# Kernel optimization log

Measured on AMD Instinct MI355X. Metric: run time of the kernel, lower is better.

The kernel has to match this reference:

```python
import jax, jax.numpy as jnp
import numpy as np

# graph layout constants
B = 64        # number of graphs
NPG = 512     # nodes per graph
N = B * NPG   # total nodes
DEG = 16      # avg degree
E = N * DEG   # total edges
F_IN = 256
H, C = 4, 64  # heads, per-head dim
K = NPG // 2  # topk pooling keeps ratio=0.5 per graph


def setup_inputs() -> dict:
    key = jax.random.key(0)
    ks = jax.random.split(key, 8)
    x = jax.random.normal(ks[0], (N, F_IN), dtype=jnp.float32)
    # within-graph random edges (src -> dst), contiguous node ids per graph
    offs = jnp.repeat(jnp.arange(B, dtype=jnp.int64) * NPG, NPG * DEG)
    src = offs + jax.random.randint(ks[1], (E,), 0, NPG)
    dst = offs + jax.random.randint(ks[2], (E,), 0, NPG)
    edge_index = jnp.stack([src, dst]).astype(jnp.int64)
    W = jax.random.normal(ks[3], (F_IN, H, C), dtype=jnp.float32) / np.sqrt(F_IN)
    att_src = jax.random.normal(ks[4], (H, C), dtype=jnp.float32) / np.sqrt(C)
    att_dst = jax.random.normal(ks[5], (H, C), dtype=jnp.float32) / np.sqrt(C)
    bias = jnp.zeros((H * C,), dtype=jnp.float32)
    bn_gamma = jnp.ones((H * C,), dtype=jnp.float32)
    bn_beta = jnp.zeros((H * C,), dtype=jnp.float32)
    pool_weight = jax.random.normal(ks[6], (H * C,), dtype=jnp.float32) / np.sqrt(H * C)
    return {"x": x, "edge_index": edge_index, "W": W, "att_src": att_src,
            "att_dst": att_dst, "bias": bias, "bn_gamma": bn_gamma,
            "bn_beta": bn_beta, "pool_weight": pool_weight}


def reference(x, edge_index, W, att_src, att_dst, bias, bn_gamma, bn_beta, pool_weight):
    n = x.shape[0]
    # --- GATConv ---
    h = jnp.einsum('nf,fhc->nhc', x, W)                 # [N,H,C]
    a_src = jnp.sum(h * att_src, axis=-1)               # [N,H]
    a_dst = jnp.sum(h * att_dst, axis=-1)               # [N,H]
    loops = jnp.arange(n, dtype=edge_index.dtype)        # add_self_loops=True default
    src = jnp.concatenate([edge_index[0], loops])
    dst = jnp.concatenate([edge_index[1], loops])
    e = jax.nn.leaky_relu(a_src[src] + a_dst[dst], 0.2)  # [E+N,H]
    # scatter-softmax over edges grouped by destination node
    emax = jax.ops.segment_max(e, dst, num_segments=n)
    ex = jnp.exp(e - emax[dst])
    den = jax.ops.segment_sum(ex, dst, num_segments=n)
    alpha = ex / (den[dst] + 1e-16)                      # [E+N,H]
    msg = alpha[:, :, None] * h[src]                     # [E+N,H,C]
    out = jax.ops.segment_sum(msg, dst, num_segments=n)  # [N,H,C]
    feat = out.reshape(n, H * C) + bias                  # concat heads
    # --- ReLU + BatchNorm (batch stats, training mode) ---
    feat = jax.nn.relu(feat)
    mean = jnp.mean(feat, axis=0)
    var = jnp.var(feat, axis=0)
    feat = (feat - mean) * jax.lax.rsqrt(var + 1e-5) * bn_gamma + bn_beta
    # --- TopKPooling (score = x.w/||w||, keep top ratio per graph, gate by tanh) ---
    score = feat @ pool_weight / jnp.linalg.norm(pool_weight)  # [N]
    top_s, top_i = jax.lax.top_k(score.reshape(B, NPG), K)     # [B,K]
    fg = feat.reshape(B, NPG, H * C)
    sel = jnp.take_along_axis(fg, top_i[:, :, None], axis=1)    # [B,K,HC]
    pooled = sel * jnp.tanh(top_s)[:, :, None]
    return pooled.reshape(B * K, H * C)
```

## Files before the change

kernel.cpp:

```cpp
#include <hip/hip_runtime.h>
#include <math.h>

#define N_NODES 32768
#define NPG 512
#define NGRAPH 64
#define KKEEP 256
#define CAP 64

typedef __attribute__((ext_vector_type(8))) short short8;
typedef __attribute__((ext_vector_type(4))) float f32x4;

__device__ __forceinline__ unsigned short f2bf(float v) {
  unsigned u = __builtin_bit_cast(unsigned, v);
  u = (u + 0x7FFFu + ((u >> 16) & 1u)) >> 16;
  return (unsigned short)u;
}
__device__ __forceinline__ float bf2f(unsigned short u) {
  unsigned v = ((unsigned)u) << 16;
  return __builtin_bit_cast(float, v);
}

__device__ __forceinline__ void async_cp16(unsigned short* l, const unsigned short* g) {
  __builtin_amdgcn_global_load_lds(
      (const __attribute__((address_space(1))) unsigned int*)g,
      (__attribute__((address_space(3))) unsigned int*)l, 16, 0, 0);
}

__device__ __forceinline__ void block_barrier() {
  __builtin_amdgcn_sched_barrier(0);
  asm volatile("s_barrier" ::: "memory");
  __builtin_amdgcn_sched_barrier(0);
}
__device__ __forceinline__ void wait_all() {
  asm volatile("s_waitcnt vmcnt(0) lgkmcnt(0)" ::: "memory");
  __builtin_amdgcn_sched_barrier(0);
}

__global__ __launch_bounds__(256) void k_conv(
    const float* __restrict__ W,
    unsigned short* __restrict__ wth, unsigned short* __restrict__ wtl,
    unsigned short* __restrict__ wtll) {
  const int t = threadIdx.x;
  int n = blockIdx.x * 4 + (t >> 6);
  int k = (t & 63) * 4;
  unsigned short hb[4], lb[4], qb[4];
#pragma unroll
  for (int j = 0; j < 4; j++) {
    float v = W[(size_t)(k + j) * 256 + n];
    unsigned short hh = f2bf(v);
    float e1 = v - bf2f(hh);
    unsigned short ll = f2bf(e1);
    float e2 = e1 - bf2f(ll);
    hb[j] = hh; lb[j] = ll; qb[j] = f2bf(e2);
  }
  *(uint2*)&wth[(size_t)n * 256 + k] = *(uint2*)&hb[0];
  *(uint2*)&wtl[(size_t)n * 256 + k] = *(uint2*)&lb[0];
  *(uint2*)&wtll[(size_t)n * 256 + k] = *(uint2*)&qb[0];
}

#define A_STR 129
#define A_SZ 12384
#define B_BASE 12384
#define B_SZ 12288
__global__ __launch_bounds__(512, 4) void k_gemm_hist(
    const float* __restrict__ x,
    const unsigned short* __restrict__ wth, const unsigned short* __restrict__ wtl,
    const unsigned short* __restrict__ wtll,
    const float* __restrict__ attS, const float* __restrict__ attD,
    float* __restrict__ h, float* __restrict__ a_src, float* __restrict__ a_dst,
    const int* __restrict__ ei, int E, int* __restrict__ cnt,
    unsigned short* __restrict__ nbr) {
  __shared__ unsigned short lds[36960];
  const int t = threadIdx.x;
  const int bid = blockIdx.x;
  if (bid >= 512) {
    int e = (bid - 512) * 512 + t;
    if (e < E) {
      int s = ei[e];
      int d = ei[E + e];
      int slot = atomicAdd(&cnt[d], 1);
      if (slot < CAP) nbr[(size_t)d * CAP + slot] = (unsigned short)(s & (NPG - 1));
    }
    return;
  }
  const int mb = (bid & 7) * 32 + (bid >> 4);
  const int nh = (bid >> 3) & 1;
  const int row0 = mb * 128;
  const int wid = t >> 6, lane = t & 63;
  const int q = lane >> 4, ln = lane & 15;
  const int wm = (wid >> 1) * 32, wn = (wid & 1) * 64;
  const int sr = t >> 2, scq = t & 3;
  f32x4 acc[2][4] = {};

  {
    size_t ga = (size_t)(row0 + sr) * 256 + scq * 8;
    float4 f0 = *(const float4*)&x[ga];
    float4 f1 = *(const float4*)&x[ga + 4];
    float ff[8] = {f0.x, f0.y, f0.z, f0.w, f1.x, f1.y, f1.z, f1.w};
    unsigned short hs[8], ls[8], qs[8];
#pragma unroll
    for (int j = 0; j < 8; j++) {
      unsigned short hh = f2bf(ff[j]);
      float e1 = ff[j] - bf2f(hh);
      unsigned short ll = f2bf(e1);
      float e2 = e1 - bf2f(ll);
      hs[j] = hh; ls[j] = ll; qs[j] = f2bf(e2);
    }
    *(uint4*)&lds[((0 * 4 + scq) * A_STR + sr) * 8] = *(uint4*)&hs[0];
    *(uint4*)&lds[((1 * 4 + scq) * A_STR + sr) * 8] = *(uint4*)&ls[0];
    *(uint4*)&lds[((2 * 4 + scq) * A_STR + sr) * 8] = *(uint4*)&qs[0];
    size_t gb = (size_t)(nh * 128 + (t & 127)) * 256 + (t >> 7) * 8;
    async_cp16(&lds[B_BASE + 0 * 4096 + t * 8], &wth[gb]);
    async_cp16(&lds[B_BASE + 1 * 4096 + t * 8], &wtl[gb]);
    async_cp16(&lds[B_BASE + 2 * 4096 + t * 8], &wtll[gb]);
  }
  wait_all();
  block_barrier();

  for (int kc = 0; kc < 8; kc++) {
    const int cur = kc & 1;
    float4 f0, f1;
    if (kc < 7) {
      const int k1 = (kc + 1) * 32;
      size_t ga = (size_t)(row0 + sr) * 256 + k1 + scq * 8;
      f0 = *(const float4*)&x[ga];
      f1 = *(const float4*)&x[ga + 4];
      unsigned short* bb = &lds[B_BASE + (cur ^ 1) * B_SZ];
      size_t gb = (size_t)(nh * 128 + (t & 127)) * 256 + k1 + (t >> 7) * 8;
      async_cp16(&bb[0 * 4096 + t * 8], &wth[gb]);
      async_cp16(&bb[1 * 4096 + t * 8], &wtl[gb]);
      async_cp16(&bb[2 * 4096 + t * 8], &wtll[gb]);
    }
    const unsigned short* bc = &lds[B_BASE + cur * B_SZ];
    short8 ah[2], al[2], aq[2];
#pragma unroll
    for (int mt = 0; mt < 2; mt++) {
      int r = wm + mt * 16 + ln;
      ah[mt] = *(const short8*)&lds[((0 * 4 + q) * A_STR + r) * 8];
      al[mt] = *(const short8*)&lds[((1 * 4 + q) * A_STR + r) * 8];
      aq[mt] = *(const short8*)&lds[((2 * 4 + q) * A_STR + r) * 8];
    }
#pragma unroll
    for (int nt = 0; nt < 4; nt++) {
      int r = wn + nt * 16 + ln;
      short8 bh = *(const short8*)&bc[0 * 4096 + (q * 128 + r) * 8];
      short8 bl = *(const short8*)&bc[1 * 4096 + (q * 128 + r) * 8];
      short8 bq = *(const short8*)&bc[2 * 4096 + (q * 128 + r) * 8];
#pragma unroll
      for (int mt = 0; mt < 2; mt++) {
        acc[mt][nt] = __builtin_amdgcn_mfma_f32_16x16x32_bf16(ah[mt], bh, acc[mt][nt], 0, 0, 0);
        acc[mt][nt] = __builtin_amdgcn_mfma_f32_16x16x32_bf16(ah[mt], bl, acc[mt][nt], 0, 0, 0);
        acc[mt][nt] = __builtin_amdgcn_mfma_f32_16x16x32_bf16(al[mt], bh, acc[mt][nt], 0, 0, 0);
        acc[mt][nt] = __builtin_amdgcn_mfma_f32_16x16x32_bf16(ah[mt], bq, acc[mt][nt], 0, 0, 0);
        acc[mt][nt] = __builtin_amdgcn_mfma_f32_16x16x32_bf16(al[mt], bl, acc[mt][nt], 0, 0, 0);
        acc[mt][nt] = __builtin_amdgcn_mfma_f32_16x16x32_bf16(aq[mt], bh, acc[mt][nt], 0, 0, 0);
      }
    }
    unsigned short hs[8], ls[8], qs[8];
    if (kc < 7) {
      float ff[8] = {f0.x, f0.y, f0.z, f0.w, f1.x, f1.y, f1.z, f1.w};
#pragma unroll
      for (int j = 0; j < 8; j++) {
        unsigned short hh = f2bf(ff[j]);
        float e1 = ff[j] - bf2f(hh);
        unsigned short ll = f2bf(e1);
        float e2 = e1 - bf2f(ll);
        hs[j] = hh; ls[j] = ll; qs[j] = f2bf(e2);
      }
    }
    block_barrier();
    if (kc < 7) {
      *(uint4*)&lds[((0 * 4 + scq) * A_STR + sr) * 8] = *(uint4*)&hs[0];
      *(uint4*)&lds[((1 * 4 + scq) * A_STR + sr) * 8] = *(uint4*)&ls[0];
      *(uint4*)&lds[((2 * 4 + scq) * A_STR + sr) * 8] = *(uint4*)&qs[0];
    }
    wait_all();
    block_barrier();
  }

  const int head = nh * 2 + (wid & 1);
  float sA[4], sD[4];
#pragma unroll
  for (int nt = 0; nt < 4; nt++) {
    int n = nh * 128 + wn + nt * 16 + ln;
    sA[nt] = attS[n];
    sD[nt] = attD[n];
  }
  float2* epi = (float2*)lds;
#pragma unroll
  for (int mt = 0; mt < 2; mt++) {
#pragma unroll
    for (int reg = 0; reg < 4; reg++) {
      int m = row0 + wm + mt * 16 + q * 4 + reg;
      float ps = 0.f, pd = 0.f;
#pragma unroll
      for (int nt = 0; nt < 4; nt++) {
        float v = acc[mt][nt][reg];
        h[(size_t)m * 256 + nh * 128 + wn + nt * 16 + ln] = v;
        ps = fmaf(v, sA[nt], ps);
        pd = fmaf(v, sD[nt], pd);
      }
      epi[(((wid * 4 + q) * 8) + mt * 4 + reg) * 18 + (ln ^ (q * 4))] =
          make_float2(ps, pd);
    }
  }
  __syncthreads();
  if (lane < 32) {
    const int rr2 = lane & 7;
    const int q2 = lane >> 3;
    const int base = (((wid * 4 + q2) * 8) + rr2) * 18;
    float ps = 0.f, pd = 0.f;
#pragma unroll
    for (int i = 0; i < 16; i++) {
      float2 v = epi[base + (i ^ (q2 * 4))];
      ps += v.x;
      pd += v.y;
    }
    int m = row0 + wm + (rr2 >> 2) * 16 + q2 * 4 + (rr2 & 3);
    a_src[m * 4 + head] = ps;
    a_dst[m * 4 + head] = pd;
  }
}

__global__ __launch_bounds__(256) void k_agg(
    const float* __restrict__ h, const float* __restrict__ a_src,
    const float* __restrict__ a_dst, const int* __restrict__ cnt,
    const unsigned short* __restrict__ nbr, const float* __restrict__ bias,
    float* __restrict__ feat) {
  __shared__ float p_lds[4][68][4];
  __shared__ int s_lds[4][68];
  const int wv = threadIdx.x >> 6;
  const int lane = threadIdx.x & 63;
  int nb = (blockIdx.x & 7) * (N_NODES / 4 / 8) + (blockIdx.x >> 3);
  const int node = nb * 4 + wv;
  const int head = lane >> 4;
  const int li = lane & 15;
  const int c0 = lane * 4;
  const int base = node & ~(NPG - 1);
  const float ad = a_dst[node * 4 + head];
  int n = cnt[node];
  if (n > CAP) n = CAP;
  float e_reg[5];
  int srcs[5];
  int nit = 0;
  float m = -1e30f;
  for (int j = li; j <= n; j += 16) {
    int s = (j < n) ? base + (int)nbr[(size_t)node * CAP + j] : node;
    float e = a_src[s * 4 + head] + ad;
    e = (e > 0.f) ? e : 0.2f * e;
    srcs[nit] = s;
    e_reg[nit++] = e;
    m = fmaxf(m, e);
  }
#pragma unroll
  for (int d = 1; d < 16; d <<= 1) m = fmaxf(m, __shfl_xor(m, d, 16));
  float l = 0.f;
  for (int i = 0; i < nit; i++) {
    int j = li + i * 16;
    float p = __expf(e_reg[i] - m);
    l += p;
    p_lds[wv][j][head] = p;
    if (head == 0) s_lds[wv][j] = srcs[i];
  }
#pragma unroll
  for (int d = 1; d < 16; d <<= 1) l += __shfl_xor(l, d, 16);
  const float linv = 1.f / (l + 1e-16f);
  __builtin_amdgcn_s_waitcnt(0);
  float4 acc0 = make_float4(0.f, 0.f, 0.f, 0.f);
  float4 acc1 = make_float4(0.f, 0.f, 0.f, 0.f);
  int j = 0;
  for (; j + 1 <= n; j += 2) {
    float p0 = p_lds[wv][j][head];
    float p1 = p_lds[wv][j + 1][head];
    int s0 = s_lds[wv][j];
    int s1 = s_lds[wv][j + 1];
    float4 h0 = *(const float4*)&h[(size_t)s0 * 256 + c0];
    float4 h1 = *(const float4*)&h[(size_t)s1 * 256 + c0];
    acc0.x = fmaf(p0, h0.x, acc0.x); acc1.x = fmaf(p1, h1.x, acc1.x);
    acc0.y = fmaf(p0, h0.y, acc0.y); acc1.y = fmaf(p1, h1.y, acc1.y);
    acc0.z = fmaf(p0, h0.z, acc0.z); acc1.z = fmaf(p1, h1.z, acc1.z);
    acc0.w = fmaf(p0, h0.w, acc0.w); acc1.w = fmaf(p1, h1.w, acc1.w);
  }
  if (j <= n) {
    float p0 = p_lds[wv][j][head];
    int s0 = s_lds[wv][j];
    float4 h0 = *(const float4*)&h[(size_t)s0 * 256 + c0];
    acc0.x = fmaf(p0, h0.x, acc0.x);
    acc0.y = fmaf(p0, h0.y, acc0.y);
    acc0.z = fmaf(p0, h0.z, acc0.z);
    acc0.w = fmaf(p0, h0.w, acc0.w);
  }
  const float4 b4 = *(const float4*)&bias[c0];
  float4 o;
  o.x = fmaxf(fmaf(acc0.x + acc1.x, linv, b4.x), 0.f);
  o.y = fmaxf(fmaf(acc0.y + acc1.y, linv, b4.y), 0.f);
  o.z = fmaxf(fmaf(acc0.z + acc1.z, linv, b4.z), 0.f);
  o.w = fmaxf(fmaf(acc0.w + acc1.w, linv, b4.w), 0.f);
  *(float4*)&feat[(size_t)node * 256 + c0] = o;
}

__global__ __launch_bounds__(256) void k_bn_partial(const float* __restrict__ feat,
                                                    double* __restrict__ psum,
                                                    double* __restrict__ psq) {
  const int c = threadIdx.x;
  const int r0 = blockIdx.x * 128;
  double s = 0.0, q = 0.0;
  for (int i = 0; i < 128; i++) {
    double v = (double)feat[(size_t)(r0 + i) * 256 + c];
    s += v;
    q += v * v;
  }
  psum[blockIdx.x * 256 + c] = s;
  psq[blockIdx.x * 256 + c] = q;
}

__global__ __launch_bounds__(1024) void k_bn_final(
    const double* __restrict__ psum, const double* __restrict__ psq,
    const float* __restrict__ gam, const float* __restrict__ bet,
    const float* __restrict__ pw, float* __restrict__ cA, float* __restrict__ cB,
    float* __restrict__ sv) {
  __shared__ double reds[4][256];
  __shared__ double redq[4][256];
  __shared__ double wsq[256];
  __shared__ double sb[256];
  const int t = threadIdx.x;
  const int c = t & 255, sl = t >> 8;
  double s = 0.0, q = 0.0;
  for (int i = sl * 64; i < sl * 64 + 64; i++) {
    s += psum[i * 256 + c];
    q += psq[i * 256 + c];
  }
  reds[sl][c] = s;
  redq[sl][c] = q;
  if (sl == 0) {
    double w = (double)pw[c];
    wsq[c] = w * w;
  }
  __syncthreads();
  if (t == 0) {
    double nn = 0.0;
    for (int i = 0; i < 256; i++) nn += wsq[i];
    wsq[0] = sqrt(nn);
  }
  __syncthreads();
  if (sl == 0) {
    s = reds[0][c] + reds[1][c] + reds[2][c] + reds[3][c];
    q = redq[0][c] + redq[1][c] + redq[2][c] + redq[3][c];
    double mean = s / (double)N_NODES;
    double var = q / (double)N_NODES - mean * mean;
    double a = (double)gam[c] / sqrt(var + 1e-5);
    double cb = (double)bet[c] - mean * a;
    cA[c] = (float)a;
    cB[c] = (float)cb;
    double pwnv = (double)pw[c] / wsq[0];
    sv[c] = (float)(a * pwnv);
    sb[c] = cb * pwnv;
  }
  __syncthreads();
  if (t == 0) {
    double s0 = 0.0;
    for (int i = 0; i < 256; i++) s0 += sb[i];
    sv[256] = (float)s0;
  }
}

__global__ __launch_bounds__(256) void k_score(
    const float* __restrict__ feat, const float* __restrict__ sv,
    float* __restrict__ score) {
  const int lane = threadIdx.x & 63;
  const int node = blockIdx.x * 4 + (threadIdx.x >> 6);
  const int c0 = lane * 4;
  float4 f = *(const float4*)&feat[(size_t)node * 256 + c0];
  float4 w = *(const float4*)&sv[c0];
  float p = f.x * w.x + f.y * w.y + f.z * w.z + f.w * w.w;
#pragma unroll
  for (int d = 1; d < 64; d <<= 1) p += __shfl_xor(p, d, 64);
  if (lane == 0) score[node] = p + sv[256];
}

__global__ __launch_bounds__(256) void k_topk(
    const float* __restrict__ score, const float* __restrict__ feat,
    const float* __restrict__ cA, const float* __restrict__ cB,
    float* __restrict__ out) {
  __shared__ float ss[NPG];
  __shared__ int rnk[64];
  __shared__ float gt[64];
  const int g = blockIdx.x >> 3;
  const int part = blockIdx.x & 7;
  const int t = threadIdx.x;
  ss[t] = score[g * NPG + t];
  ss[t + 256] = score[g * NPG + t + 256];
  __syncthreads();
  const int ln = t & 3;
  const int ndl = part * 64 + (t >> 2);
  const float s = ss[ndl];
  int rank = 0;
  for (int j = ln * 128; j < ln * 128 + 128; j++) {
    float sj = ss[j];
    rank += (sj > s || (sj == s && j < ndl)) ? 1 : 0;
  }
  rank += __shfl_xor(rank, 1);
  rank += __shfl_xor(rank, 2);
  if (ln == 0) {
    rnk[t >> 2] = rank;
    gt[t >> 2] = tanhf(s);
  }
  __syncthreads();
  for (int idx = t; idx < 64 * 64; idx += 256) {
    int r = idx >> 6;
    int rank2 = rnk[r];
    if (rank2 < KKEEP) {
      int c4 = (idx & 63) * 4;
      int node = g * NPG + part * 64 + r;
      float4 f = *(const float4*)&feat[(size_t)node * 256 + c4];
      float4 a = *(const float4*)&cA[c4];
      float4 b = *(const float4*)&cB[c4];
      float tg = gt[r];
      float4 o;
      o.x = fmaf(f.x, a.x, b.x) * tg;
      o.y = fmaf(f.y, a.y, b.y) * tg;
      o.z = fmaf(f.z, a.z, b.z) * tg;
      o.w = fmaf(f.w, a.w, b.w) * tg;
      *(float4*)&out[(size_t)(g * KKEEP + rank2) * 256 + c4] = o;
    }
  }
}

extern "C" void kernel_launch(void* const* d_in, const int* in_sizes, int n_in,
                              void* d_out, int out_size, void* d_ws, size_t ws_size,
                              hipStream_t stream) {
  const float* x    = (const float*)d_in[0];
  const int*   ei   = (const int*)d_in[1];
  const float* W    = (const float*)d_in[2];
  const float* attS = (const float*)d_in[3];
  const float* attD = (const float*)d_in[4];
  const float* bias = (const float*)d_in[5];
  const float* gam  = (const float*)d_in[6];
  const float* bet  = (const float*)d_in[7];
  const float* pw   = (const float*)d_in[8];
  float* out = (float*)d_out;
  const int E = in_sizes[1] / 2;

  char* p = (char*)d_ws;
  float* h     = (float*)p; p += (size_t)N_NODES * 256 * 4;
  float* feat  = (float*)p; p += (size_t)N_NODES * 256 * 4;
  float* a_src = (float*)p; p += (size_t)N_NODES * 4 * 4;
  float* a_dst = (float*)p; p += (size_t)N_NODES * 4 * 4;
  float* score = (float*)p; p += (size_t)N_NODES * 4;
  double* psum = (double*)p; p += (size_t)256 * 256 * 8;
  double* psq  = (double*)p; p += (size_t)256 * 256 * 8;
  float* cA    = (float*)p; p += 256 * 4;
  float* cB    = (float*)p; p += 256 * 4;
  float* sv    = (float*)p; p += 260 * 4;
  unsigned short* wth  = (unsigned short*)p; p += (size_t)256 * 256 * 2;
  unsigned short* wtl  = (unsigned short*)p; p += (size_t)256 * 256 * 2;
  unsigned short* wtll = (unsigned short*)p; p += (size_t)256 * 256 * 2;
  int* cnt     = (int*)p;   p += (size_t)N_NODES * 4;
  unsigned short* nbr = (unsigned short*)p; p += (size_t)N_NODES * CAP * 2;

  hipMemsetAsync(cnt, 0, (size_t)N_NODES * 4, stream);
  k_conv<<<64, 256, 0, stream>>>(W, wth, wtl, wtll);
  k_gemm_hist<<<1536, 512, 0, stream>>>(x, wth, wtl, wtll, attS, attD,
                                        h, a_src, a_dst, ei, E, cnt, nbr);
  k_agg<<<N_NODES / 4, 256, 0, stream>>>(h, a_src, a_dst, cnt, nbr, bias, feat);
  k_bn_partial<<<256, 256, 0, stream>>>(feat, psum, psq);
  k_bn_final<<<1, 1024, 0, stream>>>(psum, psq, gam, bet, pw, cA, cB, sv);
  k_score<<<N_NODES / 4, 256, 0, stream>>>(feat, sv, score);
  k_topk<<<NGRAPH * 8, 256, 0, stream>>>(score, feat, cA, cB, out);
}
```

Before: 203.7 us.

## Load A operand directly into registers, dropping LDS staging and a barrier

The GEMM A-operand (x rows) is no longer split into bf16 hi/lo/residual parts and staged through LDS. Each wave now loads its own x fragment straight from global memory into registers and does the three-way bf16 split there. This removes the A-tile LDS writes and reads and one block barrier per k-step, and shrinks shared memory, which may allow more blocks per CU. In exchange, the two wave columns that share rows each load and convert the same x data, so global x traffic and conversion ALU work double.

```diff
diff --git a/kernel.cpp b/kernel.cpp
--- a/kernel.cpp
+++ b/kernel.cpp
@@ -58,9 +58,6 @@
   *(uint2*)&wtll[(size_t)n * 256 + k] = *(uint2*)&qb[0];
 }
 
-#define A_STR 129
-#define A_SZ 12384
-#define B_BASE 12384
 #define B_SZ 12288
 __global__ __launch_bounds__(512, 4) void k_gemm_hist(
     const float* __restrict__ x,
@@ -70,7 +67,7 @@
     float* __restrict__ h, float* __restrict__ a_src, float* __restrict__ a_dst,
     const int* __restrict__ ei, int E, int* __restrict__ cnt,
     unsigned short* __restrict__ nbr) {
-  __shared__ unsigned short lds[36960];
+  __shared__ unsigned short lds[24576];
   const int t = threadIdx.x;
   const int bid = blockIdx.x;
   if (bid >= 512) {
@@ -89,57 +86,61 @@
   const int wid = t >> 6, lane = t & 63;
   const int q = lane >> 4, ln = lane & 15;
   const int wm = (wid >> 1) * 32, wn = (wid & 1) * 64;
-  const int sr = t >> 2, scq = t & 3;
   f32x4 acc[2][4] = {};
 
-  {
-    size_t ga = (size_t)(row0 + sr) * 256 + scq * 8;
-    float4 f0 = *(const float4*)&x[ga];
-    float4 f1 = *(const float4*)&x[ga + 4];
-    float ff[8] = {f0.x, f0.y, f0.z, f0.w, f1.x, f1.y, f1.z, f1.w};
-    unsigned short hs[8], ls[8], qs[8];
-#pragma unroll
-    for (int j = 0; j < 8; j++) {
-      unsigned short hh = f2bf(ff[j]);
-      float e1 = ff[j] - bf2f(hh);
-      unsigned short ll = f2bf(e1);
-      float e2 = e1 - bf2f(ll);
-      hs[j] = hh; ls[j] = ll; qs[j] = f2bf(e2);
-    }
-    *(uint4*)&lds[((0 * 4 + scq) * A_STR + sr) * 8] = *(uint4*)&hs[0];
-    *(uint4*)&lds[((1 * 4 + scq) * A_STR + sr) * 8] = *(uint4*)&ls[0];
-    *(uint4*)&lds[((2 * 4 + scq) * A_STR + sr) * 8] = *(uint4*)&qs[0];
-    size_t gb = (size_t)(nh * 128 + (t & 127)) * 256 + (t >> 7) * 8;
-    async_cp16(&lds[B_BASE + 0 * 4096 + t * 8], &wth[gb]);
-    async_cp16(&lds[B_BASE + 1 * 4096 + t * 8], &wtl[gb]);
-    async_cp16(&lds[B_BASE + 2 * 4096 + t * 8], &wtll[gb]);
-  }
+  const float* xr0 = &x[(size_t)(row0 + wm + ln) * 256 + q * 8];
+  const float* xr1 = &x[(size_t)(row0 + wm + 16 + ln) * 256 + q * 8];
+  const size_t gb0 = (size_t)(nh * 128 + (t & 127)) * 256 + (t >> 7) * 8;
+
+  async_cp16(&lds[0 * 4096 + t * 8], &wth[gb0]);
+  async_cp16(&lds[1 * 4096 + t * 8], &wtl[gb0]);
+  async_cp16(&lds[2 * 4096 + t * 8], &wtll[gb0]);
+  float4 cf0 = *(const float4*)(xr0);
+  float4 cf1 = *(const float4*)(xr0 + 4);
+  float4 cf2 = *(const float4*)(xr1);
+  float4 cf3 = *(const float4*)(xr1 + 4);
   wait_all();
   block_barrier();
 
   for (int kc = 0; kc < 8; kc++) {
     const int cur = kc & 1;
-    float4 f0, f1;
+    float4 nf0, nf1, nf2, nf3;
     if (kc < 7) {
       const int k1 = (kc + 1) * 32;
-      size_t ga = (size_t)(row0 + sr) * 256 + k1 + scq * 8;
-      f0 = *(const float4*)&x[ga];
-      f1 = *(const float4*)&x[ga + 4];
-      unsigned short* bb = &lds[B_BASE + (cur ^ 1) * B_SZ];
-      size_t gb = (size_t)(nh * 128 + (t & 127)) * 256 + k1 + (t >> 7) * 8;
-      async_cp16(&bb[0 * 4096 + t * 8], &wth[gb]);
-      async_cp16(&bb[1 * 4096 + t * 8], &wtl[gb]);
-      async_cp16(&bb[2 * 4096 + t * 8], &wtll[gb]);
-    }
-    const unsigned short* bc = &lds[B_BASE + cur * B_SZ];
+      unsigned short* bb = &lds[(cur ^ 1) * B_SZ];
+      async_cp16(&bb[0 * 4096 + t * 8], &wth[gb0 + k1]);
+      async_cp16(&bb[1 * 4096 + t * 8], &wtl[gb0 + k1]);
+      async_cp16(&bb[2 * 4096 + t * 8], &wtll[gb0 + k1]);
+      nf0 = *(const float4*)(xr0 + k1);
+      nf1 = *(const float4*)(xr0 + k1 + 4);
+      nf2 = *(const float4*)(xr1 + k1);
+      nf3 = *(const float4*)(xr1 + k1 + 4);
+    }
     short8 ah[2], al[2], aq[2];
 #pragma unroll
     for (int mt = 0; mt < 2; mt++) {
-      int r = wm + mt * 16 + ln;
-      ah[mt] = *(const short8*)&lds[((0 * 4 + q) * A_STR + r) * 8];
-      al[mt] = *(const short8*)&lds[((1 * 4 + q) * A_STR + r) * 8];
-      aq[mt] = *(const short8*)&lds[((2 * 4 + q) * A_STR + r) * 8];
-    }
+      float ff[8];
+      if (mt == 0) {
+        ff[0] = cf0.x; ff[1] = cf0.y; ff[2] = cf0.z; ff[3] = cf0.w;
+        ff[4] = cf1.x; ff[5] = cf1.y; ff[6] = cf1.z; ff[7] = cf1.w;
+      } else {
+        ff[0] = cf2.x; ff[1] = cf2.y; ff[2] = cf2.z; ff[3] = cf2.w;
+        ff[4] = cf3.x; ff[5] = cf3.y; ff[6] = cf3.z; ff[7] = cf3.w;
+      }
+      unsigned short hs[8], ls[8], qs[8];
+#pragma unroll
+      for (int j = 0; j < 8; j++) {
+        unsigned short hh = f2bf(ff[j]);
+        float e1 = ff[j] - bf2f(hh);
+        unsigned short ll = f2bf(e1);
+        float e2 = e1 - bf2f(ll);
+        hs[j] = hh; ls[j] = ll; qs[j] = f2bf(e2);
+      }
+      ah[mt] = *(const short8*)&hs[0];
+      al[mt] = *(const short8*)&ls[0];
+      aq[mt] = *(const short8*)&qs[0];
+    }
+    const unsigned short* bc = &lds[cur * B_SZ];
 #pragma unroll
     for (int nt = 0; nt < 4; nt++) {
       int r = wn + nt * 16 + ln;
@@ -156,26 +157,9 @@
         acc[mt][nt] = __builtin_amdgcn_mfma_f32_16x16x32_bf16(aq[mt], bh, acc[mt][nt], 0, 0, 0);
       }
     }
-    unsigned short hs[8], ls[8], qs[8];
-    if (kc < 7) {
-      float ff[8] = {f0.x, f0.y, f0.z, f0.w, f1.x, f1.y, f1.z, f1.w};
-#pragma unroll
-      for (int j = 0; j < 8; j++) {
-        unsigned short hh = f2bf(ff[j]);
-        float e1 = ff[j] - bf2f(hh);
-        unsigned short ll = f2bf(e1);
-        float e2 = e1 - bf2f(ll);
-        hs[j] = hh; ls[j] = ll; qs[j] = f2bf(e2);
-      }
-    }
-    block_barrier();
-    if (kc < 7) {
-      *(uint4*)&lds[((0 * 4 + scq) * A_STR + sr) * 8] = *(uint4*)&hs[0];
-      *(uint4*)&lds[((1 * 4 + scq) * A_STR + sr) * 8] = *(uint4*)&ls[0];
-      *(uint4*)&lds[((2 * 4 + scq) * A_STR + sr) * 8] = *(uint4*)&qs[0];
-    }
     wait_all();
     block_barrier();
+    if (kc < 7) { cf0 = nf0; cf1 = nf1; cf2 = nf2; cf3 = nf3; }
   }
 
   const int head = nh * 2 + (wid & 1);
```

Measured after the change: 220.7 us. 1.08x slower.

## Fold count memset into conversion kernel, interleave GEMM/histogram blocks, widen BN partial grid

Applied to the files above, without the earlier changes.

Zeroing of the per-node edge counter moves from a separate memset into extra blocks of the weight-conversion kernel, removing one launch. The fused GEMM+histogram kernel now interleaves its blocks (one GEMM block per three) instead of running all GEMM blocks first, so atomics-heavy histogram work overlaps with the matrix-multiply tiles across CUs. The BN partial-sum kernel is split into 1024 blocks of 64 threads for more parallelism. The interleaving also changes the GEMM tile-to-block mapping, which may affect cache locality.

```diff
diff --git a/kernel.cpp b/kernel.cpp
--- a/kernel.cpp
+++ b/kernel.cpp
@@ -39,8 +39,13 @@
 __global__ __launch_bounds__(256) void k_conv(
     const float* __restrict__ W,
     unsigned short* __restrict__ wth, unsigned short* __restrict__ wtl,
-    unsigned short* __restrict__ wtll) {
+    unsigned short* __restrict__ wtll, int* __restrict__ cnt) {
   const int t = threadIdx.x;
+  if (blockIdx.x >= 64) {
+    int i = (blockIdx.x - 64) * 1024 + t * 4;
+    *(int4*)&cnt[i] = make_int4(0, 0, 0, 0);
+    return;
+  }
   int n = blockIdx.x * 4 + (t >> 6);
   int k = (t & 63) * 4;
   unsigned short hb[4], lb[4], qb[4];
@@ -59,7 +64,6 @@
 }
 
 #define A_STR 129
-#define A_SZ 12384
 #define B_BASE 12384
 #define B_SZ 12288
 __global__ __launch_bounds__(512, 4) void k_gemm_hist(
@@ -73,8 +77,9 @@
   __shared__ unsigned short lds[36960];
   const int t = threadIdx.x;
   const int bid = blockIdx.x;
-  if (bid >= 512) {
-    int e = (bid - 512) * 512 + t;
+  if (bid % 3 != 0) {
+    int ord = bid - bid / 3 - 1;
+    int e = ord * 512 + t;
     if (e < E) {
       int s = ei[e];
       int d = ei[E + e];
@@ -83,8 +88,10 @@
     }
     return;
   }
-  const int mb = (bid & 7) * 32 + (bid >> 4);
-  const int nh = (bid >> 3) & 1;
+  const int g = bid / 3;
+  const int p = (3 * g) & 7;
+  const int mb = p * 32 + (g >> 4);
+  const int nh = (g >> 3) & 1;
   const int row0 = mb * 128;
   const int wid = t >> 6, lane = t & 63;
   const int q = lane >> 4, ln = lane & 15;
@@ -299,19 +306,20 @@
   *(float4*)&feat[(size_t)node * 256 + c0] = o;
 }
 
-__global__ __launch_bounds__(256) void k_bn_partial(const float* __restrict__ feat,
-                                                    double* __restrict__ psum,
-                                                    double* __restrict__ psq) {
-  const int c = threadIdx.x;
-  const int r0 = blockIdx.x * 128;
+__global__ __launch_bounds__(64) void k_bn_partial(const float* __restrict__ feat,
+                                                   double* __restrict__ psum,
+                                                   double* __restrict__ psq) {
+  const int chunk = blockIdx.x >> 2;
+  const int c = (blockIdx.x & 3) * 64 + threadIdx.x;
+  const int r0 = chunk * 128;
   double s = 0.0, q = 0.0;
   for (int i = 0; i < 128; i++) {
     double v = (double)feat[(size_t)(r0 + i) * 256 + c];
     s += v;
     q += v * v;
   }
-  psum[blockIdx.x * 256 + c] = s;
-  psq[blockIdx.x * 256 + c] = q;
+  psum[chunk * 256 + c] = s;
+  psq[chunk * 256 + c] = q;
 }
 
 __global__ __launch_bounds__(1024) void k_bn_final(
@@ -458,12 +466,11 @@
   int* cnt     = (int*)p;   p += (size_t)N_NODES * 4;
   unsigned short* nbr = (unsigned short*)p; p += (size_t)N_NODES * CAP * 2;
 
-  hipMemsetAsync(cnt, 0, (size_t)N_NODES * 4, stream);
-  k_conv<<<64, 256, 0, stream>>>(W, wth, wtl, wtll);
+  k_conv<<<96, 256, 0, stream>>>(W, wth, wtl, wtll, cnt);
   k_gemm_hist<<<1536, 512, 0, stream>>>(x, wth, wtl, wtll, attS, attD,
                                         h, a_src, a_dst, ei, E, cnt, nbr);
   k_agg<<<N_NODES / 4, 256, 0, stream>>>(h, a_src, a_dst, cnt, nbr, bias, feat);
-  k_bn_partial<<<256, 256, 0, stream>>>(feat, psum, psq);
+  k_bn_partial<<<1024, 64, 0, stream>>>(feat, psum, psq);
   k_bn_final<<<1, 1024, 0, stream>>>(psum, psq, gam, bet, pw, cA, cB, sv);
   k_score<<<N_NODES / 4, 256, 0, stream>>>(feat, sv, score);
   k_topk<<<NGRAPH * 8, 256, 0, stream>>>(score, feat, cA, cB, out);
```

New measurement: 213.4 us. 1.05x slower.
